# Kernel optimization log

Measured on AMD Instinct MI355X. Metric: run time of the kernel, lower is better.

The kernel has to match this reference:

```python
import jax, jax.numpy as jnp
import numpy as np

VOCAB = 21
EPS = 1e-5


def rmsnorm(x, w):
    return x * jax.lax.rsqrt(jnp.mean(x * x, axis=-1, keepdims=True) + EPS) * w


def mamba_layer(h, in_w, conv_w, conv_b, xp_w, dtp_w, dtp_b, A_log, Dp, out_w):
    # h: (B, L, D)
    Bsz, L, _ = h.shape
    di, dc = conv_w.shape
    n = A_log.shape[-1]
    r = dtp_w.shape[-1]
    xz = jnp.einsum('bld,ed->ble', h, in_w)          # (B, L, 2*di)
    xi, z = jnp.split(xz, 2, axis=-1)
    # causal depthwise conv of width dc
    xp = jnp.pad(xi, ((0, 0), (dc - 1, 0), (0, 0)))
    xc = conv_b + sum(xp[:, k:k + L, :] * conv_w[:, k] for k in range(dc))
    xc = jax.nn.silu(xc)                              # (B, L, di)
    dbc = jnp.einsum('bld,ed->ble', xc, xp_w)         # (B, L, r+2n)
    dt, Bm, Cm = dbc[..., :r], dbc[..., r:r + n], dbc[..., r + n:]
    dt = jax.nn.softplus(jnp.einsum('blr,dr->bld', dt, dtp_w) + dtp_b)  # (B, L, di)
    A = -jnp.exp(A_log)                               # (di, n)

    def step(hst, inp):
        x_t, dt_t, B_t, C_t = inp                     # (B,di),(B,di),(B,n),(B,n)
        dA = jnp.exp(dt_t[..., None] * A)             # (B, di, n)
        hst = dA * hst + (dt_t * x_t)[..., None] * B_t[:, None, :]
        y_t = jnp.einsum('bdn,bn->bd', hst, C_t)
        return hst, y_t

    h0 = jnp.zeros((Bsz, di, n), dtype=h.dtype)
    xs = (xc.swapaxes(0, 1), dt.swapaxes(0, 1), Bm.swapaxes(0, 1), Cm.swapaxes(0, 1))
    _, ys = jax.lax.scan(step, h0, xs)
    y = ys.swapaxes(0, 1) + xc * Dp                   # skip term D*x
    y = y * jax.nn.silu(z)                            # gate
    return jnp.einsum('bld,ed->ble', y, out_w)


def setup_inputs() -> dict:
    key = jax.random.key(0)
    B, L, D = 4, 1024, 512
    n_layers, n, dc, expand = 2, 16, 3, 2
    di = expand * D
    r = (D + 15) // 16  # dt_rank = ceil(d_model/16) = 32
    ks = jax.random.split(key, 12)
    f32 = jnp.float32
    inp = {}
    inp['x'] = jax.random.randint(ks[0], (B, L), 0, VOCAB)
    inp['emb'] = 0.02 * jax.random.normal(ks[1], (VOCAB, D), f32)
    inp['norm_w'] = jnp.ones((n_layers, D), f32)
    inp['in_proj_w'] = (D ** -0.5) * jax.random.normal(ks[2], (n_layers, 2 * di, D), f32)
    inp['conv_w'] = (dc ** -0.5) * jax.random.normal(ks[3], (n_layers, di, dc), f32)
    inp['conv_b'] = jnp.zeros((n_layers, di), f32)
    inp['x_proj_w'] = (di ** -0.5) * jax.random.normal(ks[4], (n_layers, r + 2 * n, di), f32)
    inp['dt_proj_w'] = (r ** -0.5) * jax.random.normal(ks[5], (n_layers, di, r), f32)
    inp['dt_proj_b'] = jax.random.uniform(ks[6], (n_layers, di), f32, minval=-4.0, maxval=-1.0)
    inp['A_log'] = jnp.log(jnp.broadcast_to(jnp.arange(1, n + 1, dtype=f32), (n_layers, di, n)))
    inp['D_param'] = jnp.ones((n_layers, di), f32)
    inp['out_proj_w'] = (di ** -0.5) * jax.random.normal(ks[7], (n_layers, D, di), f32)
    inp['fc_w'] = (D ** -0.5) * jax.random.normal(ks[8], (2, D), f32)
    inp['fc_b'] = jnp.zeros((2,), f32)
    return inp


def reference(x, emb, norm_w, in_proj_w, conv_w, conv_b, x_proj_w, dt_proj_w,
              dt_proj_b, A_log, D_param, out_proj_w, fc_w, fc_b):
    h = emb[x].astype(jnp.float32)                    # (B, L, D)
    n_layers = norm_w.shape[0]
    for l in range(n_layers):
        h = rmsnorm(
            mamba_layer(h, in_proj_w[l], conv_w[l], conv_b[l], x_proj_w[l],
                        dt_proj_w[l], dt_proj_b[l], A_log[l], D_param[l],
                        out_proj_w[l]),
            norm_w[l])
    pooled = jnp.mean(h, axis=1)                      # global_pool=True
    out = jnp.tanh(pooled)                            # dropout is identity at eval
    return out @ fc_w.T + fc_b                        # (B, 2)
```

## Files before the change

kernel.cpp:

```cpp
#include <hip/hip_runtime.h>
#include <math.h>

constexpr int Bsz = 4, Lseq = 1024, Dmodel = 512, NLAYERS = 2;
constexpr int DI = 1024, NST = 16, RNK = 32;
constexpr int BLQ = Bsz * Lseq;
constexpr int NCH = 32, CLEN = 32;

typedef __attribute__((ext_vector_type(8))) short short8v;
typedef __attribute__((ext_vector_type(8))) unsigned short ushort8v;
typedef __attribute__((ext_vector_type(4))) float f32x4;
typedef unsigned short ushort;

__device__ inline ushort bf16_rne(float v) {
  unsigned u = __float_as_uint(v);
  u += 0x7FFFu + ((u >> 16) & 1u);
  return (ushort)(u >> 16);
}
__device__ inline float bf2f(ushort u) {
  return __uint_as_float(((unsigned)u) << 16);
}
__device__ inline size_t frag_off(int row, int k, int KT) {
  int kt = k >> 6, kk = (k >> 5) & 1, k8 = (k >> 3) & 3;
  int lanei = (row & 15) | (k8 << 4), msub = (row >> 4) & 7, rt = row >> 7;
  return ((((size_t)(rt * KT + kt) * 2 + kk) * 8 + msub) * 64 + lanei) * 8;
}
#define GLDS(gp, lp) __builtin_amdgcn_global_load_lds( \
    (const __attribute__((address_space(1))) void*)(gp), \
    (__attribute__((address_space(3))) void*)(lp), 16, 0, 0)

__global__ __launch_bounds__(256) void embcvt_kernel(
    const int* __restrict__ x, const float* __restrict__ emb,
    const float* __restrict__ in_w, const float* __restrict__ xp_w,
    const float* __restrict__ out_w,
    ushort* __restrict__ Af,
    ushort* __restrict__ WIh, ushort* __restrict__ WIl,
    ushort* __restrict__ XPh, ushort* __restrict__ XPl,
    ushort* __restrict__ WOh)
{
  int blk = blockIdx.x;
  if (blk < 1024) {
    int i = blk * 256 + threadIdx.x;
    int row = i >> 6, k = (i & 63) * 8;
    int tok = x[row];
    const float* src = &emb[(size_t)tok * Dmodel + k];
    float4 v0 = *reinterpret_cast<const float4*>(src);
    float4 v1 = *reinterpret_cast<const float4*>(src + 4);
    float xs[8] = {v0.x, v0.y, v0.z, v0.w, v1.x, v1.y, v1.z, v1.w};
    ushort hv[8];
#pragma unroll
    for (int e = 0; e < 8; ++e) hv[e] = bf16_rne(xs[e]);
    *reinterpret_cast<ushort8v*>(&Af[frag_off(row, k, 8)]) =
        *reinterpret_cast<ushort8v*>(hv);
    return;
  }
  const float* src; ushort *dh, *dl; size_t doff; bool wantlo = true;
  if (blk < 2048) {
    int u = (blk - 1024) * 256 + threadIdx.x;
    int l = u >> 17, rem = u & 131071;
    int row = rem >> 6, k = (rem & 63) * 8;
    src = in_w + (size_t)l * 2048 * 512 + (size_t)row * 512 + k;
    size_t base = (size_t)l * 2048 * 512;
    dh = WIh + base; dl = WIl + base; doff = frag_off(row, k, 8);
  } else if (blk < 2112) {
    int u = (blk - 2048) * 256 + threadIdx.x;
    int l = u >> 13, rem = u & 8191;
    int row = rem >> 7, k = (rem & 127) * 8;
    src = xp_w + (size_t)l * 64 * 1024 + (size_t)row * 1024 + k;
    size_t base = (size_t)l * 131072;
    dh = XPh + base; dl = XPl + base; doff = frag_off(row, k, 16);
  } else {
    int u = (blk - 2112) * 256 + threadIdx.x;
    int l = u >> 16, rem = u & 65535;
    int row = rem >> 7, k = (rem & 127) * 8;
    src = out_w + (size_t)l * 512 * 1024 + (size_t)row * 1024 + k;
    size_t base = (size_t)l * 512 * 1024;
    dh = WOh + base; dl = nullptr; doff = frag_off(row, k, 16); wantlo = false;
  }
  float4 v0 = *reinterpret_cast<const float4*>(src);
  float4 v1 = *reinterpret_cast<const float4*>(src + 4);
  float xs[8] = {v0.x, v0.y, v0.z, v0.w, v1.x, v1.y, v1.z, v1.w};
  ushort hs[8], ls[8];
#pragma unroll
  for (int j = 0; j < 8; ++j) {
    unsigned u = __float_as_uint(xs[j]);
    float hf = __uint_as_float(u & 0xFFFF0000u);
    float r = xs[j] - hf;
    hs[j] = (ushort)(u >> 16);
    ls[j] = (ushort)(__float_as_uint(r) >> 16);
  }
  *reinterpret_cast<ushort8v*>(&dh[doff]) = *reinterpret_cast<ushort8v*>(hs);
  if (wantlo)
    *reinterpret_cast<ushort8v*>(&dl[doff]) = *reinterpret_cast<ushort8v*>(ls);
}

__global__ __launch_bounds__(256) void gemm_in_mfma(
    const ushort* __restrict__ Ah,
    const ushort* __restrict__ Bh, const ushort* __restrict__ Bl,
    ushort* __restrict__ C)
{
  extern __shared__ ushort smu[];
  constexpr int AOFF = 0, BHOFF = 4096, BLOFF = 20480;
  const int tid = threadIdx.x, lane = tid & 63, wid = tid >> 6;
  const int bn = blockIdx.x, bm = blockIdx.y;
  const int bm0 = bm * 64;
  const int rtA = bm0 >> 7, half = (bm0 >> 6) & 1;
  f32x4 acc[4][4];
#pragma unroll
  for (int i = 0; i < 4; ++i)
#pragma unroll
    for (int j = 0; j < 4; ++j) acc[i][j] = (f32x4){0.f, 0.f, 0.f, 0.f};
  const int rtB = wid >> 1;
  const int nsub = (wid & 1) * 4;

  for (int kt = 0; kt < 8; ++kt) {
    if (wid == 0) {
      const ushort* cb = Ah + ((size_t)(rtA * 8 + kt)) * 8192;
#pragma unroll
      for (int kk = 0; kk < 2; ++kk)
#pragma unroll
        for (int m = 0; m < 4; ++m)
          GLDS(cb + (kk * 8 + half * 4 + m) * 512 + lane * 8,
               smu + AOFF + (kk * 4 + m) * 512);
    } else if (wid == 1) {
#pragma unroll
      for (int rt = 0; rt < 2; ++rt) {
        const ushort* cb = Bh + ((size_t)((bn * 2 + rt) * 8 + kt)) * 8192;
#pragma unroll
        for (int i = 0; i < 16; ++i)
          GLDS(cb + i * 512 + lane * 8, smu + BHOFF + rt * 8192 + i * 512);
      }
    } else if (wid == 2) {
#pragma unroll
      for (int rt = 0; rt < 2; ++rt) {
        const ushort* cb = Bl + ((size_t)((bn * 2 + rt) * 8 + kt)) * 8192;
#pragma unroll
        for (int i = 0; i < 16; ++i)
          GLDS(cb + i * 512 + lane * 8, smu + BLOFF + rt * 8192 + i * 512);
      }
    }
    __syncthreads();
#pragma unroll
    for (int kk = 0; kk < 2; ++kk) {
      short8v a[4], b[4];
#pragma unroll
      for (int i = 0; i < 4; ++i)
        a[i] = *reinterpret_cast<const short8v*>(&smu[AOFF + ((kk * 4 + i) * 64 + lane) * 8]);
#pragma unroll
      for (int j = 0; j < 4; ++j)
        b[j] = *reinterpret_cast<const short8v*>(
            &smu[BHOFF + rtB * 8192 + ((kk * 8 + nsub + j) * 64 + lane) * 8]);
#pragma unroll
      for (int ms = 0; ms < 4; ++ms)
#pragma unroll
        for (int ns = 0; ns < 4; ++ns)
          acc[ms][ns] = __builtin_amdgcn_mfma_f32_16x16x32_bf16(a[ms], b[ns], acc[ms][ns], 0, 0, 0);
#pragma unroll
      for (int j = 0; j < 4; ++j)
        b[j] = *reinterpret_cast<const short8v*>(
            &smu[BLOFF + rtB * 8192 + ((kk * 8 + nsub + j) * 64 + lane) * 8]);
#pragma unroll
      for (int ms = 0; ms < 4; ++ms)
#pragma unroll
        for (int ns = 0; ns < 4; ++ns)
          acc[ms][ns] = __builtin_amdgcn_mfma_f32_16x16x32_bf16(a[ms], b[ns], acc[ms][ns], 0, 0, 0);
    }
    __syncthreads();
  }
  const int cr = lane >> 4, cc = lane & 15;
#pragma unroll
  for (int ms = 0; ms < 4; ++ms) {
    int row0 = bm0 + ms * 16 + cr * 4;
#pragma unroll
    for (int ns = 0; ns < 4; ++ns) {
      int col = bn * 256 + wid * 64 + ns * 16 + cc;
#pragma unroll
      for (int r = 0; r < 4; ++r)
        C[(size_t)(row0 + r) * 2048 + col] = bf16_rne(acc[ms][ns][r]);
    }
  }
}

__global__ __launch_bounds__(256) void gemm_out_mfma(
    const ushort* __restrict__ Ah, const ushort* __restrict__ Bh,
    float* __restrict__ P)
{
  constexpr int ASZ = 8192;
  __shared__ ushort lds[2 * ASZ];
  const int tid = threadIdx.x, lane = tid & 63, wid = tid >> 6;
  const int wm = wid >> 1, wn = wid & 1;
  const int bm = blockIdx.y, bn = blockIdx.x, z = blockIdx.z;
  f32x4 acc[4][4];
#pragma unroll
  for (int i = 0; i < 4; ++i)
#pragma unroll
    for (int j = 0; j < 4; ++j) acc[i][j] = (f32x4){0.f, 0.f, 0.f, 0.f};
  const int msel = wm * 4, nsel = wn * 4;
  for (int kt = z * 8; kt < z * 8 + 8; ++kt) {
    if (wid == 0) {
      const ushort* cb = Ah + ((size_t)(bm * 16 + kt)) * 8192;
#pragma unroll
      for (int i = 0; i < 16; ++i)
        GLDS(cb + i * 512 + lane * 8, lds + i * 512);
    } else if (wid == 1) {
      const ushort* cb = Bh + ((size_t)(bn * 16 + kt)) * 8192;
#pragma unroll
      for (int i = 0; i < 16; ++i)
        GLDS(cb + i * 512 + lane * 8, lds + ASZ + i * 512);
    }
    __syncthreads();
#pragma unroll
    for (int kk = 0; kk < 2; ++kk) {
      short8v a[4], b[4];
#pragma unroll
      for (int i = 0; i < 4; ++i) {
        a[i] = *reinterpret_cast<const short8v*>(&lds[((kk * 8 + msel + i) * 64 + lane) * 8]);
        b[i] = *reinterpret_cast<const short8v*>(&lds[ASZ + ((kk * 8 + nsel + i) * 64 + lane) * 8]);
      }
#pragma unroll
      for (int ms = 0; ms < 4; ++ms)
#pragma unroll
        for (int ns = 0; ns < 4; ++ns)
          acc[ms][ns] = __builtin_amdgcn_mfma_f32_16x16x32_bf16(a[ms], b[ns], acc[ms][ns], 0, 0, 0);
    }
    __syncthreads();
  }
  float* Pz = P + (size_t)z * BLQ * Dmodel;
  const int cr = lane >> 4, cc = lane & 15;
#pragma unroll
  for (int ms = 0; ms < 4; ++ms) {
    int row0 = bm * 128 + (msel + ms) * 16 + cr * 4;
#pragma unroll
    for (int ns = 0; ns < 4; ++ns) {
      int col = bn * 128 + (nsel + ns) * 16 + cc;
#pragma unroll
      for (int r = 0; r < 4; ++r)
        Pz[(size_t)(row0 + r) * Dmodel + col] = acc[ms][ns][r];
    }
  }
}

__global__ __launch_bounds__(256) void convxp_kernel(
    const ushort* __restrict__ XZb, const float* __restrict__ cw,
    const float* __restrict__ cb,
    const ushort* __restrict__ XPh, const ushort* __restrict__ XPl,
    float* __restrict__ XC, float* __restrict__ P)
{
  constexpr int XZOFF = 0;
  constexpr int AOFF  = 1312;
  constexpr int BHOFF = 2336;
  constexpr int BLOFF = 6432;
  __shared__ ushort smu[10528];
  const int tid = threadIdx.x, lane = tid & 63, wid = tid >> 6;
  const int cr = lane >> 4, cc = lane & 15;
  const int bm0 = blockIdx.x * 16;
  const int z = blockIdx.y;
  const int batchbase = bm0 & ~(Lseq - 1);
  f32x4 acc = (f32x4){0.f, 0.f, 0.f, 0.f};

  for (int kt = z * 8; kt < z * 8 + 8; ++kt) {
    const int kcol0 = kt * 64;
    if (wid < 2) {
#pragma unroll
      for (int i = 0; i < 2; ++i) {
        int u = tid + i * 128;
        if (u < 144) {
          int r = u >> 3, c8 = u & 7;
          int grow = bm0 - 2 + r;
          ushort8v v = {};
          if (grow >= batchbase)
            v = *reinterpret_cast<const ushort8v*>(
                &XZb[(size_t)grow * 2048 + kcol0 + c8 * 8]);
          *reinterpret_cast<ushort8v*>(&smu[XZOFF + r * 72 + c8 * 8]) = v;
        }
      }
    } else {
      const ushort* src = ((wid == 2) ? XPh : XPl) + (size_t)kt * 8192 + lane * 8;
      int dst0 = (wid == 2) ? BHOFF : BLOFF;
#pragma unroll
      for (int i = 0; i < 8; ++i) {
        int sidx = (i >> 2) * 8 + (i & 3);
        GLDS(src + sidx * 512, smu + dst0 + i * 512);
      }
    }
    __syncthreads();
    if (tid < 128) {
      int row = tid >> 3, c8 = tid & 7;
      int d0 = kcol0 + c8 * 8;
      ushort8v cur = *reinterpret_cast<ushort8v*>(&smu[XZOFF + (row + 2) * 72 + c8 * 8]);
      ushort8v pm1 = *reinterpret_cast<ushort8v*>(&smu[XZOFF + (row + 1) * 72 + c8 * 8]);
      ushort8v pm2 = *reinterpret_cast<ushort8v*>(&smu[XZOFF + (row + 0) * 72 + c8 * 8]);
      float wv[24], bv[8];
#pragma unroll
      for (int q = 0; q < 6; ++q)
        *reinterpret_cast<float4*>(&wv[q * 4]) =
            *reinterpret_cast<const float4*>(&cw[d0 * 3 + q * 4]);
      *reinterpret_cast<float4*>(&bv[0]) = *reinterpret_cast<const float4*>(&cb[d0]);
      *reinterpret_cast<float4*>(&bv[4]) = *reinterpret_cast<const float4*>(&cb[d0 + 4]);
      float os[8]; ushort hv[8];
#pragma unroll
      for (int e = 0; e < 8; ++e) {
        float a = bv[e];
        a = fmaf(bf2f(pm2[e]), wv[e * 3 + 0], a);
        a = fmaf(bf2f(pm1[e]), wv[e * 3 + 1], a);
        a = fmaf(bf2f(cur[e]), wv[e * 3 + 2], a);
        float s = a / (1.f + __expf(-a));
        os[e] = s; hv[e] = bf16_rne(s);
      }
      float* op = &XC[(size_t)(bm0 + row) * DI + d0];
      *reinterpret_cast<float4*>(op) = *reinterpret_cast<float4*>(&os[0]);
      *reinterpret_cast<float4*>(op + 4) = *reinterpret_cast<float4*>(&os[4]);
      int kk = c8 >> 2, k8 = c8 & 3;
      int idx = (kk * 64 + (row | (k8 << 4))) ^ k8;
      *reinterpret_cast<ushort8v*>(&smu[AOFF + idx * 8]) =
          *reinterpret_cast<ushort8v*>(hv);
    }
    __syncthreads();
#pragma unroll
    for (int kk = 0; kk < 2; ++kk) {
      int aidx = (kk * 64 + lane) ^ ((lane >> 4) & 3);
      short8v a = *reinterpret_cast<const short8v*>(&smu[AOFF + aidx * 8]);
      short8v bh = *reinterpret_cast<const short8v*>(&smu[BHOFF + ((kk * 4 + wid) * 64 + lane) * 8]);
      short8v bl = *reinterpret_cast<const short8v*>(&smu[BLOFF + ((kk * 4 + wid) * 64 + lane) * 8]);
      acc = __builtin_amdgcn_mfma_f32_16x16x32_bf16(a, bh, acc, 0, 0, 0);
      acc = __builtin_amdgcn_mfma_f32_16x16x32_bf16(a, bl, acc, 0, 0, 0);
    }
    __syncthreads();
  }
  float* Pz = P + (size_t)z * BLQ * 64;
#pragma unroll
  for (int r = 0; r < 4; ++r)
    Pz[(size_t)(bm0 + cr * 4 + r) * 64 + wid * 16 + cc] = acc[r];
}

__global__ __launch_bounds__(256) void xpost_kernel(
    const float* __restrict__ P, const float* __restrict__ dtw,
    const float* __restrict__ dtb, float* __restrict__ DTb,
    float* __restrict__ BCc)
{
  const int tid = threadIdx.x;
  const size_t SL = (size_t)BLQ * 64;
  if (blockIdx.y == 16) {
    int i0 = blockIdx.x * 4096 + tid;
#pragma unroll
    for (int i = 0; i < 16; ++i) {
      int idx = i0 + i * 256;
      int bt = idx >> 5, n = idx & 31;
      size_t g = (size_t)bt * 64 + 32 + n;
      BCc[idx] = P[g] + P[SL + g];
    }
    return;
  }
  const int dg = blockIdx.y, bm0 = blockIdx.x * 128;
  __shared__ float db[128][33];
  __shared__ float wt[64][33];
#pragma unroll
  for (int i = 0; i < 16; ++i) {
    int e = tid + i * 256;
    int r = e >> 5, c = e & 31;
    size_t g = (size_t)(bm0 + r) * 64 + c;
    db[r][c] = P[g] + P[SL + g];
  }
#pragma unroll
  for (int i = 0; i < 8; ++i) {
    int e = tid + i * 256;
    int r = e >> 5, c = e & 31;
    wt[r][c] = dtw[(size_t)(dg * 64 + r) * 32 + c];
  }
  __syncthreads();
  const int d_loc = tid & 63, wv = tid >> 6;
  const float bias = dtb[dg * 64 + d_loc];
#pragma unroll 4
  for (int i = 0; i < 32; ++i) {
    int r = wv + i * 4;
    float dot = 0.f;
#pragma unroll
    for (int c = 0; c < 32; ++c) dot = fmaf(db[r][c], wt[d_loc][c], dot);
    float v = dot + bias;
    DTb[(size_t)(bm0 + r) * DI + dg * 64 + d_loc] =
        (v > 15.f) ? v : log1pf(__expf(v));
  }
}

__global__ __launch_bounds__(256) void scan_p1_kernel(
    const float* __restrict__ DTb, const float* __restrict__ XC,
    const float* __restrict__ BCc, const float* __restrict__ Alog,
    float* __restrict__ HEND, float* __restrict__ DSUM)
{
  const int d = blockIdx.x * 256 + threadIdx.x;
  const int c = blockIdx.y, b = blockIdx.z;
  const int t0 = b * Lseq + c * CLEN;
  __shared__ float Bs[CLEN][16];
#pragma unroll
  for (int i = 0; i < 2; ++i) {
    int e = threadIdx.x + i * 256;
    Bs[e >> 4][e & 15] = BCc[(size_t)(t0 + (e >> 4)) * 32 + (e & 15)];
  }
  float An[16];
#pragma unroll
  for (int j = 0; j < 4; ++j) {
    float4 a = *reinterpret_cast<const float4*>(&Alog[d * 16 + j * 4]);
    An[j * 4 + 0] = -__expf(a.x); An[j * 4 + 1] = -__expf(a.y);
    An[j * 4 + 2] = -__expf(a.z); An[j * 4 + 3] = -__expf(a.w);
  }
  __syncthreads();
  float h[16] = {};
  float S = 0.f;
  for (int t = 0; t < CLEN; ++t) {
    size_t g = (size_t)(t0 + t) * DI + d;
    float dt = DTb[g], xc = XC[g];
    S += dt;
    float dtxc = dt * xc;
#pragma unroll
    for (int n = 0; n < 16; ++n)
      h[n] = fmaf(__expf(An[n] * dt), h[n], dtxc * Bs[t][n]);
  }
  size_t hb = ((size_t)(b * NCH + c) * DI + d) * 16;
#pragma unroll
  for (int j = 0; j < 4; ++j)
    *reinterpret_cast<float4*>(&HEND[hb + j * 4]) =
        *reinterpret_cast<float4*>(&h[j * 4]);
  DSUM[(size_t)(b * NCH + c) * DI + d] = S;
}

__global__ __launch_bounds__(256) void scan_p2_kernel(
    float* __restrict__ HEND, const float* __restrict__ DSUM,
    const float* __restrict__ Alog)
{
  int id = blockIdx.x * 256 + threadIdx.x;
  int n = id & 15, d = (id >> 4) & (DI - 1), b = id >> 14;
  float An = -__expf(Alog[d * 16 + n]);
  float hg = 0.f;
  for (int c = 0; c < NCH; ++c) {
    size_t hi = ((size_t)(b * NCH + c) * DI + d) * 16 + n;
    float hl = HEND[hi];
    float Dc = DSUM[(size_t)(b * NCH + c) * DI + d];
    HEND[hi] = hg;
    hg = fmaf(__expf(An * Dc), hg, hl);
  }
}

__global__ __launch_bounds__(256) void scan_p3_kernel(
    const float* __restrict__ XC, const float* __restrict__ DTb,
    const float* __restrict__ BCc, const ushort* __restrict__ XZb,
    const float* __restrict__ HEND, const float* __restrict__ Alog,
    const float* __restrict__ Dp, ushort* __restrict__ Af)
{
  const int tid = threadIdx.x;
  const int dg = blockIdx.x, c = blockIdx.y, b = blockIdx.z;
  const int d = dg * 256 + tid;
  const int t0 = b * Lseq + c * CLEN;
  __shared__ float BC[CLEN][32];
  __shared__ float ys[CLEN][264];
#pragma unroll
  for (int i = 0; i < 4; ++i) {
    int e = tid + i * 256;
    BC[e >> 5][e & 31] = BCc[(size_t)(t0 + (e >> 5)) * 32 + (e & 31)];
  }
  float An[16], h[16];
  size_t hb = ((size_t)(b * NCH + c) * DI + d) * 16;
#pragma unroll
  for (int j = 0; j < 4; ++j) {
    float4 a = *reinterpret_cast<const float4*>(&Alog[d * 16 + j * 4]);
    An[j * 4 + 0] = -__expf(a.x); An[j * 4 + 1] = -__expf(a.y);
    An[j * 4 + 2] = -__expf(a.z); An[j * 4 + 3] = -__expf(a.w);
    *reinterpret_cast<float4*>(&h[j * 4]) =
        *reinterpret_cast<const float4*>(&HEND[hb + j * 4]);
  }
  float Dpv = Dp[d];
  __syncthreads();
  for (int t = 0; t < CLEN; ++t) {
    size_t g = (size_t)(t0 + t) * DI + d;
    float dt = DTb[g], xc = XC[g];
    float z = bf2f(XZb[(size_t)(t0 + t) * (2 * DI) + DI + d]);
    float dtxc = dt * xc;
    float y = 0.f;
#pragma unroll
    for (int n = 0; n < 16; ++n) {
      h[n] = fmaf(__expf(An[n] * dt), h[n], dtxc * BC[t][n]);
      y = fmaf(h[n], BC[t][16 + n], y);
    }
    float sil = z / (1.f + __expf(-z));
    ys[t][tid] = (y + xc * Dpv) * sil;
  }
  __syncthreads();
#pragma unroll
  for (int i = 0; i < 4; ++i) {
    int u = tid + i * 256;
    int tt = u >> 5, j8 = u & 31;
    int row = t0 + tt;
    int kg = dg * 256 + j8 * 8;
    ushort hv[8];
#pragma unroll
    for (int e = 0; e < 8; ++e) hv[e] = bf16_rne(ys[tt][j8 * 8 + e]);
    *reinterpret_cast<ushort8v*>(&Af[frag_off(row, kg, 16)]) =
        *reinterpret_cast<ushort8v*>(hv);
  }
}

__global__ __launch_bounds__(256) void rmsnorm_kernel(const float* __restrict__ X,
    const float* __restrict__ W, float* __restrict__ O, ushort* __restrict__ Af) {
  int row = blockIdx.x * 4 + (threadIdx.x >> 6);
  int lane = threadIdx.x & 63;
  int k = lane * 8;
  const size_t SL = (size_t)BLQ * Dmodel;
  size_t idx = (size_t)row * Dmodel + k;
  float4 a0 = *reinterpret_cast<const float4*>(&X[idx]);
  float4 a1 = *reinterpret_cast<const float4*>(&X[idx + 4]);
  float4 b0 = *reinterpret_cast<const float4*>(&X[SL + idx]);
  float4 b1 = *reinterpret_cast<const float4*>(&X[SL + idx + 4]);
  float vs[8] = {a0.x + b0.x, a0.y + b0.y, a0.z + b0.z, a0.w + b0.w,
                 a1.x + b1.x, a1.y + b1.y, a1.z + b1.z, a1.w + b1.w};
  float ss = 0.f;
#pragma unroll
  for (int e = 0; e < 8; ++e) ss = fmaf(vs[e], vs[e], ss);
#pragma unroll
  for (int o = 32; o >= 1; o >>= 1) ss += __shfl_xor(ss, o);
  float sc = rsqrtf(ss * (1.f / Dmodel) + 1e-5f);
  const float* wp = W + k;
  float4 w0 = *reinterpret_cast<const float4*>(wp);
  float4 w1 = *reinterpret_cast<const float4*>(wp + 4);
  float wsv[8] = {w0.x, w0.y, w0.z, w0.w, w1.x, w1.y, w1.z, w1.w};
  float os[8];
  ushort hv[8];
#pragma unroll
  for (int e = 0; e < 8; ++e) {
    os[e] = vs[e] * sc * wsv[e];
    hv[e] = bf16_rne(os[e]);
  }
  float* op = O + idx;
  *reinterpret_cast<float4*>(op) = *reinterpret_cast<float4*>(&os[0]);
  *reinterpret_cast<float4*>(op + 4) = *reinterpret_cast<float4*>(&os[4]);
  *reinterpret_cast<ushort8v*>(&Af[frag_off(row, k, 8)]) =
      *reinterpret_cast<ushort8v*>(hv);
}

__global__ __launch_bounds__(256) void pool_part_kernel(const float* __restrict__ H,
    float* __restrict__ part) {
  int b = blockIdx.x, dg = blockIdx.y, tc = blockIdx.z;
  int tid = threadIdx.x;
  int d = dg * 128 + (tid & 127);
  int ph = tid >> 7;
  const float* base = H + ((size_t)(b * Lseq + tc * 128 + ph * 64)) * Dmodel + d;
  float s = 0.f;
#pragma unroll 8
  for (int t = 0; t < 64; ++t) s += base[(size_t)t * Dmodel];
  __shared__ float red[256];
  red[tid] = s; __syncthreads();
  if (ph == 0)
    part[(size_t)(b * 8 + tc) * Dmodel + d] = red[tid] + red[tid + 128];
}

__global__ __launch_bounds__(256) void pool_head_kernel(
    const float* __restrict__ part, const float* __restrict__ fcw,
    const float* __restrict__ fcb, float* __restrict__ out) {
  int b = blockIdx.x >> 1, j = blockIdx.x & 1;
  int tid = threadIdx.x;
  float s = 0.f;
  for (int d = tid; d < Dmodel; d += 256) {
    float p = 0.f;
#pragma unroll
    for (int tc = 0; tc < 8; ++tc) p += part[(size_t)(b * 8 + tc) * Dmodel + d];
    s += tanhf(p * (1.f / Lseq)) * fcw[j * Dmodel + d];
  }
#pragma unroll
  for (int o = 32; o >= 1; o >>= 1) s += __shfl_xor(s, o);
  __shared__ float w[4];
  if ((tid & 63) == 0) w[tid >> 6] = s;
  __syncthreads();
  if (tid == 0) out[b * 2 + j] = w[0] + w[1] + w[2] + w[3] + fcb[j];
}

extern "C" void kernel_launch(void* const* d_in, const int* in_sizes, int n_in,
                              void* d_out, int out_size, void* d_ws, size_t ws_size,
                              hipStream_t stream) {
  const int*   x      = (const int*)d_in[0];
  const float* emb    = (const float*)d_in[1];
  const float* norm_w = (const float*)d_in[2];
  const float* in_w   = (const float*)d_in[3];
  const float* conv_w = (const float*)d_in[4];
  const float* conv_b = (const float*)d_in[5];
  const float* xp_w   = (const float*)d_in[6];
  const float* dtp_w  = (const float*)d_in[7];
  const float* dtp_b  = (const float*)d_in[8];
  const float* A_log  = (const float*)d_in[9];
  const float* Dp     = (const float*)d_in[10];
  const float* out_w  = (const float*)d_in[11];
  const float* fc_w   = (const float*)d_in[12];
  const float* fc_b   = (const float*)d_in[13];
  float* out = (float*)d_out;

  char* p = (char*)d_ws;
  auto alloc = [&](size_t bytes) { char* r = p; p += (bytes + 255) & ~255ull; return r; };
  ushort* XZb  = (ushort*)alloc((size_t)BLQ * 2 * DI * 2);
  float*  XC   = (float*) alloc((size_t)BLQ * DI * 4);
  float*  DTb  = (float*) alloc((size_t)BLQ * DI * 4);
  float*  BCc  = (float*) alloc((size_t)BLQ * 32 * 4);
  float*  DBCP = (float*) alloc((size_t)2 * BLQ * 64 * 4);
  float*  HEND = (float*) alloc((size_t)Bsz * NCH * DI * 16 * 4);
  float*  DSUM = (float*) alloc((size_t)Bsz * NCH * DI * 4);
  float*  H    = (float*) alloc((size_t)BLQ * Dmodel * 4);
  float*  H2P  = (float*) alloc((size_t)2 * BLQ * Dmodel * 4);
  float*  PPART= (float*) alloc((size_t)Bsz * 8 * Dmodel * 4);
  ushort* AhI  = (ushort*)alloc((size_t)BLQ * Dmodel * 2);
  ushort* AhO  = (ushort*)alloc((size_t)BLQ * DI * 2);
  ushort* WIh  = (ushort*)alloc((size_t)2 * 2048 * 512 * 2);
  ushort* WIl  = (ushort*)alloc((size_t)2 * 2048 * 512 * 2);
  ushort* XPh  = (ushort*)alloc((size_t)2 * 131072 * 2);
  ushort* XPl  = (ushort*)alloc((size_t)2 * 131072 * 2);
  ushort* WOh  = (ushort*)alloc((size_t)2 * 512 * 1024 * 2);

  embcvt_kernel<<<2624, 256, 0, stream>>>(x, emb, in_w, xp_w, out_w,
      AhI, WIh, WIl, XPh, XPl, WOh);

  for (int l = 0; l < NLAYERS; ++l) {
    const float* cw  = conv_w + (size_t)l * DI * 3;
    const float* cb  = conv_b + (size_t)l * DI;
    const float* dtw = dtp_w + (size_t)l * DI * RNK;
    const float* dtb = dtp_b + (size_t)l * DI;
    const float* Al  = A_log + (size_t)l * DI * NST;
    const float* dpl = Dp    + (size_t)l * DI;
    const float* nw  = norm_w + (size_t)l * Dmodel;
    const ushort* wih = WIh + (size_t)l * 2048 * 512;
    const ushort* wil = WIl + (size_t)l * 2048 * 512;
    const ushort* xph = XPh + (size_t)l * 131072;
    const ushort* xpl = XPl + (size_t)l * 131072;
    const ushort* woh = WOh + (size_t)l * 512 * 1024;

    gemm_in_mfma<<<dim3(8, 64), 256, 73728, stream>>>(AhI, wih, wil, XZb);

    convxp_kernel<<<dim3(BLQ / 16, 2), 256, 0, stream>>>(XZb, cw, cb, xph, xpl,
        XC, DBCP);

    xpost_kernel<<<dim3(32, 17), 256, 0, stream>>>(DBCP, dtw, dtb, DTb, BCc);

    scan_p1_kernel<<<dim3(DI / 256, NCH, Bsz), 256, 0, stream>>>(
        DTb, XC, BCc, Al, HEND, DSUM);
    scan_p2_kernel<<<Bsz * DI * NST / 256, 256, 0, stream>>>(HEND, DSUM, Al);
    scan_p3_kernel<<<dim3(DI / 256, NCH, Bsz), 256, 0, stream>>>(
        XC, DTb, BCc, XZb, HEND, Al, dpl, AhO);

    gemm_out_mfma<<<dim3(4, 32, 2), 256, 0, stream>>>(AhO, woh, H2P);

    rmsnorm_kernel<<<BLQ / 4, 256, 0, stream>>>(H2P, nw, H, AhI);
  }

  pool_part_kernel<<<dim3(Bsz, Dmodel / 128, 8), 256, 0, stream>>>(H, PPART);
  pool_head_kernel<<<2 * Bsz, 256, 0, stream>>>(PPART, fc_w, fc_b, out);
}
```

Before: 279.0 us.

## Use four-way split-K in out-proj and x-proj GEMMs, fuse pooling into final RMSNorm

The out-projection and conv/x-projection kernels now split K four ways instead of two, doubling grid parallelism while adding more partial-sum buffers that the downstream rmsnorm and xpost kernels sum. The last layer's rmsnorm gains a template variant that reduces each block's four rows into per-block pooling partials. This drops the full fp32 hidden-state write and the separate pool_part kernel. pool_head then sums 256 block partials per channel, which adds more partial traffic and a longer serial loop in a tiny kernel.

```diff
diff --git a/kernel.cpp b/kernel.cpp
--- a/kernel.cpp
+++ b/kernel.cpp
@@ -195,7 +195,7 @@
 #pragma unroll
     for (int j = 0; j < 4; ++j) acc[i][j] = (f32x4){0.f, 0.f, 0.f, 0.f};
   const int msel = wm * 4, nsel = wn * 4;
-  for (int kt = z * 8; kt < z * 8 + 8; ++kt) {
+  for (int kt = z * 4; kt < z * 4 + 4; ++kt) {
     if (wid == 0) {
       const ushort* cb = Ah + ((size_t)(bm * 16 + kt)) * 8192;
 #pragma unroll
@@ -257,7 +257,7 @@
   const int batchbase = bm0 & ~(Lseq - 1);
   f32x4 acc = (f32x4){0.f, 0.f, 0.f, 0.f};
 
-  for (int kt = z * 8; kt < z * 8 + 8; ++kt) {
+  for (int kt = z * 4; kt < z * 4 + 4; ++kt) {
     const int kcol0 = kt * 64;
     if (wid < 2) {
 #pragma unroll
@@ -346,7 +346,7 @@
       int idx = i0 + i * 256;
       int bt = idx >> 5, n = idx & 31;
       size_t g = (size_t)bt * 64 + 32 + n;
-      BCc[idx] = P[g] + P[SL + g];
+      BCc[idx] = (P[g] + P[SL + g]) + (P[2 * SL + g] + P[3 * SL + g]);
     }
     return;
   }
@@ -358,7 +358,7 @@
     int e = tid + i * 256;
     int r = e >> 5, c = e & 31;
     size_t g = (size_t)(bm0 + r) * 64 + c;
-    db[r][c] = P[g] + P[SL + g];
+    db[r][c] = (P[g] + P[SL + g]) + (P[2 * SL + g] + P[3 * SL + g]);
   }
 #pragma unroll
   for (int i = 0; i < 8; ++i) {
@@ -497,19 +497,27 @@
   }
 }
 
+template<int LAST>
 __global__ __launch_bounds__(256) void rmsnorm_kernel(const float* __restrict__ X,
-    const float* __restrict__ W, float* __restrict__ O, ushort* __restrict__ Af) {
-  int row = blockIdx.x * 4 + (threadIdx.x >> 6);
-  int lane = threadIdx.x & 63;
+    const float* __restrict__ W, ushort* __restrict__ Af, float* __restrict__ PP) {
+  __shared__ float pr[4][512];
+  int w = threadIdx.x >> 6, lane = threadIdx.x & 63;
+  int row = blockIdx.x * 4 + w;
   int k = lane * 8;
   const size_t SL = (size_t)BLQ * Dmodel;
   size_t idx = (size_t)row * Dmodel + k;
-  float4 a0 = *reinterpret_cast<const float4*>(&X[idx]);
-  float4 a1 = *reinterpret_cast<const float4*>(&X[idx + 4]);
-  float4 b0 = *reinterpret_cast<const float4*>(&X[SL + idx]);
-  float4 b1 = *reinterpret_cast<const float4*>(&X[SL + idx + 4]);
-  float vs[8] = {a0.x + b0.x, a0.y + b0.y, a0.z + b0.z, a0.w + b0.w,
-                 a1.x + b1.x, a1.y + b1.y, a1.z + b1.z, a1.w + b1.w};
+  float vs[8];
+#pragma unroll
+  for (int h = 0; h < 2; ++h) {
+    float4 a = *reinterpret_cast<const float4*>(&X[idx + h * 4]);
+    float4 b = *reinterpret_cast<const float4*>(&X[SL + idx + h * 4]);
+    float4 c = *reinterpret_cast<const float4*>(&X[2 * SL + idx + h * 4]);
+    float4 d = *reinterpret_cast<const float4*>(&X[3 * SL + idx + h * 4]);
+    vs[h * 4 + 0] = (a.x + b.x) + (c.x + d.x);
+    vs[h * 4 + 1] = (a.y + b.y) + (c.y + d.y);
+    vs[h * 4 + 2] = (a.z + b.z) + (c.z + d.z);
+    vs[h * 4 + 3] = (a.w + b.w) + (c.w + d.w);
+  }
   float ss = 0.f;
 #pragma unroll
   for (int e = 0; e < 8; ++e) ss = fmaf(vs[e], vs[e], ss);
@@ -521,45 +529,38 @@
   float4 w1 = *reinterpret_cast<const float4*>(wp + 4);
   float wsv[8] = {w0.x, w0.y, w0.z, w0.w, w1.x, w1.y, w1.z, w1.w};
   float os[8];
-  ushort hv[8];
-#pragma unroll
-  for (int e = 0; e < 8; ++e) {
-    os[e] = vs[e] * sc * wsv[e];
-    hv[e] = bf16_rne(os[e]);
-  }
-  float* op = O + idx;
-  *reinterpret_cast<float4*>(op) = *reinterpret_cast<float4*>(&os[0]);
-  *reinterpret_cast<float4*>(op + 4) = *reinterpret_cast<float4*>(&os[4]);
-  *reinterpret_cast<ushort8v*>(&Af[frag_off(row, k, 8)]) =
-      *reinterpret_cast<ushort8v*>(hv);
-}
-
-__global__ __launch_bounds__(256) void pool_part_kernel(const float* __restrict__ H,
-    float* __restrict__ part) {
-  int b = blockIdx.x, dg = blockIdx.y, tc = blockIdx.z;
-  int tid = threadIdx.x;
-  int d = dg * 128 + (tid & 127);
-  int ph = tid >> 7;
-  const float* base = H + ((size_t)(b * Lseq + tc * 128 + ph * 64)) * Dmodel + d;
-  float s = 0.f;
-#pragma unroll 8
-  for (int t = 0; t < 64; ++t) s += base[(size_t)t * Dmodel];
-  __shared__ float red[256];
-  red[tid] = s; __syncthreads();
-  if (ph == 0)
-    part[(size_t)(b * 8 + tc) * Dmodel + d] = red[tid] + red[tid + 128];
+#pragma unroll
+  for (int e = 0; e < 8; ++e) os[e] = vs[e] * sc * wsv[e];
+  if (LAST == 0) {
+    ushort hv[8];
+#pragma unroll
+    for (int e = 0; e < 8; ++e) hv[e] = bf16_rne(os[e]);
+    *reinterpret_cast<ushort8v*>(&Af[frag_off(row, k, 8)]) =
+        *reinterpret_cast<ushort8v*>(hv);
+  } else {
+#pragma unroll
+    for (int e = 0; e < 8; ++e) pr[w][k + e] = os[e];
+    __syncthreads();
+#pragma unroll
+    for (int i = 0; i < 2; ++i) {
+      int d = threadIdx.x + i * 256;
+      PP[(size_t)d * 1024 + blockIdx.x] =
+          (pr[0][d] + pr[1][d]) + (pr[2][d] + pr[3][d]);
+    }
+  }
 }
 
 __global__ __launch_bounds__(256) void pool_head_kernel(
-    const float* __restrict__ part, const float* __restrict__ fcw,
+    const float* __restrict__ PP, const float* __restrict__ fcw,
     const float* __restrict__ fcb, float* __restrict__ out) {
   int b = blockIdx.x >> 1, j = blockIdx.x & 1;
   int tid = threadIdx.x;
   float s = 0.f;
   for (int d = tid; d < Dmodel; d += 256) {
+    const float* pp = PP + (size_t)d * 1024 + b * 256;
     float p = 0.f;
-#pragma unroll
-    for (int tc = 0; tc < 8; ++tc) p += part[(size_t)(b * 8 + tc) * Dmodel + d];
+#pragma unroll 8
+    for (int blk = 0; blk < 256; ++blk) p += pp[blk];
     s += tanhf(p * (1.f / Lseq)) * fcw[j * Dmodel + d];
   }
 #pragma unroll
@@ -595,12 +596,11 @@
   float*  XC   = (float*) alloc((size_t)BLQ * DI * 4);
   float*  DTb  = (float*) alloc((size_t)BLQ * DI * 4);
   float*  BCc  = (float*) alloc((size_t)BLQ * 32 * 4);
-  float*  DBCP = (float*) alloc((size_t)2 * BLQ * 64 * 4);
+  float*  DBCP = (float*) alloc((size_t)4 * BLQ * 64 * 4);
   float*  HEND = (float*) alloc((size_t)Bsz * NCH * DI * 16 * 4);
   float*  DSUM = (float*) alloc((size_t)Bsz * NCH * DI * 4);
-  float*  H    = (float*) alloc((size_t)BLQ * Dmodel * 4);
-  float*  H2P  = (float*) alloc((size_t)2 * BLQ * Dmodel * 4);
-  float*  PPART= (float*) alloc((size_t)Bsz * 8 * Dmodel * 4);
+  float*  H2P  = (float*) alloc((size_t)4 * BLQ * Dmodel * 4);
+  float*  PP   = (float*) alloc((size_t)Dmodel * 1024 * 4);
   ushort* AhI  = (ushort*)alloc((size_t)BLQ * Dmodel * 2);
   ushort* AhO  = (ushort*)alloc((size_t)BLQ * DI * 2);
   ushort* WIh  = (ushort*)alloc((size_t)2 * 2048 * 512 * 2);
@@ -628,7 +628,7 @@
 
     gemm_in_mfma<<<dim3(8, 64), 256, 73728, stream>>>(AhI, wih, wil, XZb);
 
-    convxp_kernel<<<dim3(BLQ / 16, 2), 256, 0, stream>>>(XZb, cw, cb, xph, xpl,
+    convxp_kernel<<<dim3(BLQ / 16, 4), 256, 0, stream>>>(XZb, cw, cb, xph, xpl,
         XC, DBCP);
 
     xpost_kernel<<<dim3(32, 17), 256, 0, stream>>>(DBCP, dtw, dtb, DTb, BCc);
@@ -639,11 +639,13 @@
     scan_p3_kernel<<<dim3(DI / 256, NCH, Bsz), 256, 0, stream>>>(
         XC, DTb, BCc, XZb, HEND, Al, dpl, AhO);
 
-    gemm_out_mfma<<<dim3(4, 32, 2), 256, 0, stream>>>(AhO, woh, H2P);
-
-    rmsnorm_kernel<<<BLQ / 4, 256, 0, stream>>>(H2P, nw, H, AhI);
-  }
-
-  pool_part_kernel<<<dim3(Bsz, Dmodel / 128, 8), 256, 0, stream>>>(H, PPART);
-  pool_head_kernel<<<2 * Bsz, 256, 0, stream>>>(PPART, fc_w, fc_b, out);
-}
+    gemm_out_mfma<<<dim3(4, 32, 4), 256, 0, stream>>>(AhO, woh, H2P);
+
+    if (l == NLAYERS - 1)
+      rmsnorm_kernel<1><<<BLQ / 4, 256, 0, stream>>>(H2P, nw, nullptr, PP);
+    else
+      rmsnorm_kernel<0><<<BLQ / 4, 256, 0, stream>>>(H2P, nw, AhI, nullptr);
+  }
+
+  pool_head_kernel<<<2 * Bsz, 256, 0, stream>>>(PP, fc_w, fc_b, out);
+}
```

Measured after the change: 286.3 us. +2.6%, slower.
